# Performance work log

Measured on AMD Instinct MI355X. Metric: run time of the kernel, lower is better.

Reference implementation:

```python
import math
import jax, jax.numpy as jnp
import numpy as np

ALPH = 0.8

def setup_inputs() -> dict:
    key = jax.random.key(0)
    k1, k2 = jax.random.split(key)
    B, C, N, T = 64, 64, 500, 48
    x = jax.random.normal(k1, (B, C, N, T), dtype=jnp.float32)
    s = jax.random.uniform(k2, (N, N), dtype=jnp.float32)
    return {"x": x, "s": s}

def reference(x, s):
    # x: [B, C, N, T], s: [N, N]
    B, C, N, T = x.shape
    # Row sums of the (never materialized) [N*T, N*T] supra-laplacian:
    # block row i, node v -> s.sum(axis=1)[v] + (T-1-i)*alph
    s_rowsum = s.sum(axis=1)                              # [N]
    time_term = (T - 1 - jnp.arange(T, dtype=jnp.float32)) * ALPH  # [T]
    rowsum = (time_term[:, None] + s_rowsum[None, :]).reshape(-1)  # [T*N], k = i*N+v
    # Faithful to original: x flattened as [B, C, N*T] (k = n*T + t), multiplied
    # elementwise by rowsum[k] (the 'bcn,nm->bcn' einsum reduces to this).
    x_window = x.reshape(B, C, N * T)
    x_window = jax.nn.relu(x_window * rowsum / math.sqrt(C))
    adj_dyn = jax.nn.softmax(x_window, axis=-1)            # [B, C, N*T]
    x_w_s = adj_dyn.reshape(B, C, N, T).sum(-1)            # [B, C, N]
    gram = jnp.einsum('bcn,bcm->bnm', x_w_s, x_w_s)        # [B, N, N]
    A_l = jax.nn.softmax(jax.nn.relu(gram) / math.sqrt(C), axis=-1)
    return A_l
```

## Files before the change

kernel.cpp:

```cpp
#include <hip/hip_runtime.h>
#include <math.h>

#define NN 500
#define TT 48
#define NT 24000
#define NF4 6000

typedef float f4v __attribute__((ext_vector_type(4)));

__global__ void k_srow(const float* __restrict__ s, float* __restrict__ srow) {
    int r = blockIdx.x;
    int l = threadIdx.x;
    float v = 0.f;
    for (int j = l; j < NN; j += 64) v += s[r * NN + j];
    #pragma unroll
    for (int o = 32; o; o >>= 1) v += __shfl_xor(v, o);
    if (l == 0) srow[r] = v;
}

__launch_bounds__(256, 4)
__global__ void k_p1(const float* __restrict__ x, const float* __restrict__ srow,
                     float* __restrict__ xraw, float* __restrict__ mz) {
    __shared__ float p[3072];
    __shared__ __align__(16) float sr[512];
    __shared__ __align__(16) float stg[4][2][768];
    int bid = blockIdx.x;
    int bc = bid >> 1, half = bid & 1;
    int tid = threadIdx.x;
    int w = tid >> 6, l = tid & 63;
    int fl0 = w * 768 + l;
    int rowb = half * 3072 + w * 768;

    sr[tid] = srow[(tid < NN) ? tid : (NN - 1)];
    int t2 = tid + 256;
    sr[t2] = (t2 < NN) ? srow[t2] : 0.f;
    __syncthreads();

    const f4v* xp = (const f4v*)x + (size_t)bc * NF4;

#define STAGE(s) do {                                                         \
        _Pragma("unroll")                                                     \
        for (int k_ = 0; k_ < 3; k_++) {                                      \
            int f_ = rowb + (s) * 192 + k_ * 64 + l;                          \
            int fc_ = (f_ < NF4) ? f_ : (NF4 - 1);                            \
            __builtin_amdgcn_global_load_lds(                                 \
                (const __attribute__((address_space(1))) void*)(xp + fc_),    \
                (__attribute__((address_space(3))) void*)&stg[w][(s) & 1][k_ * 256], \
                16, 0, 0);                                                    \
        }                                                                     \
    } while (0)

#define VMCNT(n) do {                                                         \
        asm volatile("s_waitcnt vmcnt(" #n ")" ::: "memory");                 \
        __builtin_amdgcn_sched_barrier(0);                                    \
    } while (0)

    float sf[12], ml[12];
    float m = 0.f;

#define COMPU(s) do {                                                         \
        _Pragma("unroll")                                                     \
        for (int k_ = 0; k_ < 3; k_++) {                                      \
            int i_ = 3 * (s) + k_;                                            \
            int f_ = rowb + (s) * 192 + k_ * 64 + l;                          \
            int fc_ = (f_ < NF4) ? f_ : (NF4 - 1);                            \
            float msk_ = (f_ < NF4) ? 1.f : 0.f;                              \
            float4 xv = ((const float4*)stg[w][(s) & 1])[k_ * 64 + l];        \
            int kk_ = 4 * fc_;                                                \
            int ti_ = kk_ / 500;                                              \
            int v_  = kk_ - ti_ * 500;                                        \
            float tt_ = (float)(TT - 1 - ti_) * 0.8f;                         \
            float4 sv = *(const float4*)(sr + v_);                            \
            float y0 = fmaxf(xv.x * (tt_ + sv.x) * 0.125f, 0.f);              \
            float y1 = fmaxf(xv.y * (tt_ + sv.y) * 0.125f, 0.f);              \
            float y2 = fmaxf(xv.z * (tt_ + sv.z) * 0.125f, 0.f);              \
            float y3 = fmaxf(xv.w * (tt_ + sv.w) * 0.125f, 0.f);              \
            float mm_ = fmaxf(fmaxf(y0, y1), fmaxf(y2, y3));                  \
            float sfi_ = __expf(y0 - mm_) + __expf(y1 - mm_)                  \
                       + __expf(y2 - mm_) + __expf(y3 - mm_);                 \
            sf[i_] = sfi_ * msk_;                                             \
            ml[i_] = mm_;                                                     \
            m = fmaxf(m, mm_);                                                \
        }                                                                     \
    } while (0)

    STAGE(0);
    STAGE(1);
    VMCNT(3);  COMPU(0);
    STAGE(2);
    VMCNT(3);  COMPU(1);
    STAGE(3);
    VMCNT(3);  COMPU(2);
    VMCNT(0);  COMPU(3);

#undef STAGE
#undef VMCNT
#undef COMPU

    #pragma unroll
    for (int o = 32; o; o >>= 1) m = fmaxf(m, __shfl_xor(m, o));

    float tot = 0.f;
    #pragma unroll
    for (int i = 0; i < 12; i++) {
        float cf = sf[i] * __expf(ml[i] - m);
        p[fl0 + i * 64] = cf;
        tot += cf;
    }
    #pragma unroll
    for (int o = 32; o; o >>= 1) tot += __shfl_xor(tot, o);

    asm volatile("s_waitcnt lgkmcnt(0)" ::: "memory");
    __builtin_amdgcn_sched_barrier(0);

    int n = half * 256 + w * 64 + l;
    if (n < NN) {
        const float4* pp = (const float4*)(p + w * 768 + l * 12);
        float4 a = pp[0], b4 = pp[1], c4 = pp[2];
        float sn = a.x + a.y + a.z + a.w + b4.x + b4.y + b4.z + b4.w
                 + c4.x + c4.y + c4.z + c4.w;
        xraw[(size_t)bc * NN + n] = sn;
    }
    if (l == 0) {
        int wv = half * 4 + w;
        mz[((size_t)bc * 8 + wv) * 2 + 0] = m;
        mz[((size_t)bc * 8 + wv) * 2 + 1] = tot;
    }
}

__global__ void k_mz(const float* __restrict__ mz, float* __restrict__ factor) {
    int bc = blockIdx.x * 256 + threadIdx.x;
    float Mw[8], Zw[8];
    float M = 0.f;
    #pragma unroll
    for (int wv = 0; wv < 8; wv++) {
        Mw[wv] = mz[((size_t)bc * 8 + wv) * 2 + 0];
        Zw[wv] = mz[((size_t)bc * 8 + wv) * 2 + 1];
        M = fmaxf(M, Mw[wv]);
    }
    float Z = 0.f;
    float e[8];
    #pragma unroll
    for (int wv = 0; wv < 8; wv++) {
        e[wv] = __expf(Mw[wv] - M);
        Z += Zw[wv] * e[wv];
    }
    float invZ = 1.f / Z;
    #pragma unroll
    for (int wv = 0; wv < 8; wv++)
        factor[(size_t)bc * 8 + wv] = e[wv] * invZ;
}

__launch_bounds__(512, 4)
__global__ void k_p2(const float* __restrict__ xraw, const float* __restrict__ factor,
                     float* __restrict__ out) {
    __shared__ __align__(16) float Xs[32 * NN + 16];
    int b = blockIdx.y;
    int rt8 = blockIdx.x;
    int tid = threadIdx.x;

    int rt = tid >> 6, cx = tid & 63;
    int r0 = rt8 * 64 + rt * 8;
    int cb0 = cx * 4, cb1 = cx * 4 + 256;

    float acc[8][8];
    #pragma unroll
    for (int i = 0; i < 8; i++)
        #pragma unroll
        for (int j = 0; j < 8; j++) acc[i][j] = 0.f;

    for (int cbk = 0; cbk < 2; cbk++) {
        const float4* src4 = (const float4*)(xraw + ((size_t)b * 64 + 32 * cbk) * NN);
        const float* fac = factor + ((size_t)b * 64 + 32 * cbk) * 8;
        __syncthreads();
        #pragma unroll
        for (int i = 0; i < 8; i++) {
            int idx = tid + i * 512;
            if (idx < 4000) {
                int c = idx / 125;
                int n4 = idx - c * 125;
                float fct = fac[c * 8 + (n4 >> 4)];
                float4 v = src4[idx];
                v.x *= fct; v.y *= fct; v.z *= fct; v.w *= fct;
                ((float4*)Xs)[idx] = v;
            }
        }
        if (tid < 16) Xs[32 * NN + tid] = 0.f;
        __syncthreads();

        #pragma unroll 4
        for (int c = 0; c < 32; c++) {
            const float* row = Xs + c * NN;
            float4 a0 = *(const float4*)(row + r0);
            float4 a1 = *(const float4*)(row + r0 + 4);
            float4 b0 = *(const float4*)(row + cb0);
            float4 b1 = *(const float4*)(row + cb1);
            float av[8] = {a0.x, a0.y, a0.z, a0.w, a1.x, a1.y, a1.z, a1.w};
            float bv[8] = {b0.x, b0.y, b0.z, b0.w, b1.x, b1.y, b1.z, b1.w};
            #pragma unroll
            for (int i = 0; i < 8; i++)
                #pragma unroll
                for (int j = 0; j < 8; j++)
                    acc[i][j] = fmaf(av[i], bv[j], acc[i][j]);
        }
    }

    bool c1v = (cx <= 60);
    size_t ob = (size_t)b * (NN * NN);
    #pragma unroll 1
    for (int ri = 0; ri < 8; ri++) {
        int r = r0 + ri;
        if (r >= NN) break;
        float u[8];
        #pragma unroll
        for (int j = 0; j < 8; j++) u[j] = fmaxf(acc[ri][j], 0.f) * 0.125f;
        float mx = fmaxf(fmaxf(u[0], u[1]), fmaxf(u[2], u[3]));
        if (c1v) mx = fmaxf(mx, fmaxf(fmaxf(u[4], u[5]), fmaxf(u[6], u[7])));
        #pragma unroll
        for (int o = 32; o; o >>= 1) mx = fmaxf(mx, __shfl_xor(mx, o));

        float e[8];
        float es = 0.f;
        #pragma unroll
        for (int j = 0; j < 4; j++) { e[j] = __expf(u[j] - mx); es += e[j]; }
        if (c1v) {
            #pragma unroll
            for (int j = 4; j < 8; j++) { e[j] = __expf(u[j] - mx); es += e[j]; }
        }
        #pragma unroll
        for (int o = 32; o; o >>= 1) es += __shfl_xor(es, o);
        float inv = 1.f / es;

        float4 w0 = make_float4(e[0] * inv, e[1] * inv, e[2] * inv, e[3] * inv);
        *(float4*)(out + ob + (size_t)r * NN + cb0) = w0;
        if (c1v) {
            float4 w1 = make_float4(e[4] * inv, e[5] * inv, e[6] * inv, e[7] * inv);
            *(float4*)(out + ob + (size_t)r * NN + cb1) = w1;
        }
    }
}

extern "C" void kernel_launch(void* const* d_in, const int* in_sizes, int n_in,
                              void* d_out, int out_size, void* d_ws, size_t ws_size,
                              hipStream_t stream) {
    const float* x = (const float*)d_in[0];
    const float* s = (const float*)d_in[1];
    float* out = (float*)d_out;
    float* wsf = (float*)d_ws;

    float* srow   = wsf;
    float* xraw   = wsf + 32768;
    float* mz     = wsf + 32768 + 2048000;
    float* factor = wsf + 32768 + 2048000 + 65536;

    k_srow<<<NN, 64, 0, stream>>>(s, srow);
    k_p1<<<64 * 64 * 2, 256, 0, stream>>>(x, srow, xraw, mz);
    k_mz<<<16, 256, 0, stream>>>(mz, factor);
    dim3 g2(8, 64);
    k_p2<<<g2, 512, 0, stream>>>(xraw, factor, out);
}
```

Measured before the change: 165.3 us.

## Make k_p1 persistent with cross-unit prefetch of the next work unit

The main pass now launches 1024 blocks instead of 8192, and each block loops over 8 work units strided by 1024. The first two stages of the next unit are issued before the current unit's epilogue, with vmcnt thresholds adjusted to match. The aim is to hide global-load latency across unit boundaries and cut block launch and setup overhead such as the srow LDS fill. In exchange there are fewer blocks to spread across CUs, and the epilogue reuses LDS that must stay consistent with the in-flight loads.

Measured after the change: 169.0 us. 2.2% more time.

```diff
diff --git a/kernel.cpp b/kernel.cpp
--- a/kernel.cpp
+++ b/kernel.cpp
@@ -24,27 +24,28 @@
     __shared__ float p[3072];
     __shared__ __align__(16) float sr[512];
     __shared__ __align__(16) float stg[4][2][768];
-    int bid = blockIdx.x;
-    int bc = bid >> 1, half = bid & 1;
+    int g = blockIdx.x;
     int tid = threadIdx.x;
     int w = tid >> 6, l = tid & 63;
     int fl0 = w * 768 + l;
-    int rowb = half * 3072 + w * 768;
 
     sr[tid] = srow[(tid < NN) ? tid : (NN - 1)];
     int t2 = tid + 256;
     sr[t2] = (t2 < NN) ? srow[t2] : 0.f;
     __syncthreads();
 
-    const f4v* xp = (const f4v*)x + (size_t)bc * NF4;
-
-#define STAGE(s) do {                                                         \
+#define SB() __builtin_amdgcn_sched_barrier(0)
+
+#define STAGE(U, s) do {                                                      \
+        int bcS_ = (U) >> 1;                                                  \
+        int rowbS_ = ((U) & 1) * 3072 + w * 768;                              \
+        const f4v* xpS_ = (const f4v*)x + (size_t)bcS_ * NF4;                 \
         _Pragma("unroll")                                                     \
         for (int k_ = 0; k_ < 3; k_++) {                                      \
-            int f_ = rowb + (s) * 192 + k_ * 64 + l;                          \
+            int f_ = rowbS_ + (s) * 192 + k_ * 64 + l;                        \
             int fc_ = (f_ < NF4) ? f_ : (NF4 - 1);                            \
             __builtin_amdgcn_global_load_lds(                                 \
-                (const __attribute__((address_space(1))) void*)(xp + fc_),    \
+                (const __attribute__((address_space(1))) void*)(xpS_ + fc_),  \
                 (__attribute__((address_space(3))) void*)&stg[w][(s) & 1][k_ * 256], \
                 16, 0, 0);                                                    \
         }                                                                     \
@@ -55,14 +56,14 @@
         __builtin_amdgcn_sched_barrier(0);                                    \
     } while (0)
 
-    float sf[12], ml[12];
-    float m = 0.f;
-
-#define COMPU(s) do {                                                         \
+    float sf[12], ml[12], m;
+
+#define COMPU(U, s) do {                                                      \
+        int rowbC_ = ((U) & 1) * 3072 + w * 768;                              \
         _Pragma("unroll")                                                     \
         for (int k_ = 0; k_ < 3; k_++) {                                      \
             int i_ = 3 * (s) + k_;                                            \
-            int f_ = rowb + (s) * 192 + k_ * 64 + l;                          \
+            int f_ = rowbC_ + (s) * 192 + k_ * 64 + l;                        \
             int fc_ = (f_ < NF4) ? f_ : (NF4 - 1);                            \
             float msk_ = (f_ < NF4) ? 1.f : 0.f;                              \
             float4 xv = ((const float4*)stg[w][(s) & 1])[k_ * 64 + l];        \
@@ -84,48 +85,75 @@
         }                                                                     \
     } while (0)
 
-    STAGE(0);
-    STAGE(1);
-    VMCNT(3);  COMPU(0);
-    STAGE(2);
-    VMCNT(3);  COMPU(1);
-    STAGE(3);
-    VMCNT(3);  COMPU(2);
-    VMCNT(0);  COMPU(3);
-
+#define EPIL(U) do {                                                          \
+        _Pragma("unroll")                                                     \
+        for (int o_ = 32; o_; o_ >>= 1) m = fmaxf(m, __shfl_xor(m, o_));      \
+        float tot_ = 0.f;                                                     \
+        _Pragma("unroll")                                                     \
+        for (int i_ = 0; i_ < 12; i_++) {                                     \
+            float cf_ = sf[i_] * __expf(ml[i_] - m);                          \
+            p[fl0 + i_ * 64] = cf_;                                           \
+            tot_ += cf_;                                                      \
+        }                                                                     \
+        _Pragma("unroll")                                                     \
+        for (int o_ = 32; o_; o_ >>= 1) tot_ += __shfl_xor(tot_, o_);         \
+        asm volatile("s_waitcnt lgkmcnt(0)" ::: "memory");                    \
+        __builtin_amdgcn_sched_barrier(0);                                    \
+        int bcE_ = (U) >> 1, halfE_ = (U) & 1;                                \
+        int n_ = halfE_ * 256 + w * 64 + l;                                   \
+        if (n_ < NN) {                                                        \
+            const float4* pp_ = (const float4*)(p + w * 768 + l * 12);        \
+            float4 a_ = pp_[0], b_ = pp_[1], c_ = pp_[2];                     \
+            float sn_ = a_.x + a_.y + a_.z + a_.w + b_.x + b_.y + b_.z + b_.w \
+                      + c_.x + c_.y + c_.z + c_.w;                            \
+            xraw[(size_t)bcE_ * NN + n_] = sn_;                               \
+        }                                                                     \
+        if (l == 0) {                                                         \
+            int wv_ = halfE_ * 4 + w;                                         \
+            mz[((size_t)bcE_ * 8 + wv_) * 2 + 0] = m;                         \
+            mz[((size_t)bcE_ * 8 + wv_) * 2 + 1] = tot_;                      \
+        }                                                                     \
+    } while (0)
+
+    int U = g;
+    STAGE(U, 0);
+    STAGE(U, 1);
+
+    {
+        int Un = U + 1024;
+        m = 0.f;
+        VMCNT(3); COMPU(U, 0); SB(); STAGE(U, 2);
+        VMCNT(3); COMPU(U, 1); SB(); STAGE(U, 3);
+        VMCNT(3); COMPU(U, 2); SB(); STAGE(Un, 0);
+        VMCNT(3); COMPU(U, 3); SB(); STAGE(Un, 1);
+        EPIL(U);
+        U = Un;
+    }
+    #pragma unroll 1
+    for (int it = 1; it < 7; ++it) {
+        int Un = U + 1024;
+        m = 0.f;
+        VMCNT(5); COMPU(U, 0); SB(); STAGE(U, 2);
+        VMCNT(5); COMPU(U, 1); SB(); STAGE(U, 3);
+        VMCNT(3); COMPU(U, 2); SB(); STAGE(Un, 0);
+        VMCNT(3); COMPU(U, 3); SB(); STAGE(Un, 1);
+        EPIL(U);
+        U = Un;
+    }
+    {
+        m = 0.f;
+        VMCNT(5); COMPU(U, 0); SB(); STAGE(U, 2);
+        VMCNT(5); COMPU(U, 1); SB(); STAGE(U, 3);
+        VMCNT(3); COMPU(U, 2);
+        VMCNT(0); COMPU(U, 3);
+        EPIL(U);
+    }
+
+#undef SB
 #undef STAGE
 #undef VMCNT
 #undef COMPU
-
-    #pragma unroll
-    for (int o = 32; o; o >>= 1) m = fmaxf(m, __shfl_xor(m, o));
-
-    float tot = 0.f;
-    #pragma unroll
-    for (int i = 0; i < 12; i++) {
-        float cf = sf[i] * __expf(ml[i] - m);
-        p[fl0 + i * 64] = cf;
-        tot += cf;
-    }
-    #pragma unroll
-    for (int o = 32; o; o >>= 1) tot += __shfl_xor(tot, o);
-
-    asm volatile("s_waitcnt lgkmcnt(0)" ::: "memory");
-    __builtin_amdgcn_sched_barrier(0);
-
-    int n = half * 256 + w * 64 + l;
-    if (n < NN) {
-        const float4* pp = (const float4*)(p + w * 768 + l * 12);
-        float4 a = pp[0], b4 = pp[1], c4 = pp[2];
-        float sn = a.x + a.y + a.z + a.w + b4.x + b4.y + b4.z + b4.w
-                 + c4.x + c4.y + c4.z + c4.w;
-        xraw[(size_t)bc * NN + n] = sn;
-    }
-    if (l == 0) {
-        int wv = half * 4 + w;
-        mz[((size_t)bc * 8 + wv) * 2 + 0] = m;
-        mz[((size_t)bc * 8 + wv) * 2 + 1] = tot;
-    }
+#undef EPIL
 }
 
 __global__ void k_mz(const float* __restrict__ mz, float* __restrict__ factor) {
@@ -254,7 +282,7 @@
     float* factor = wsf + 32768 + 2048000 + 65536;
 
     k_srow<<<NN, 64, 0, stream>>>(s, srow);
-    k_p1<<<64 * 64 * 2, 256, 0, stream>>>(x, srow, xraw, mz);
+    k_p1<<<1024, 256, 0, stream>>>(x, srow, xraw, mz);
     k_mz<<<16, 256, 0, stream>>>(mz, factor);
     dim3 g2(8, 64);
     k_p2<<<g2, 512, 0, stream>>>(xraw, factor, out);
```
